# Performance work log

Measured on AMD Instinct MI355X. Metric: run time of the kernel, lower is better.

## Reference

```python
import jax, jax.numpy as jnp
import numpy as np

DIMS, K_SIZE, V_SIZE, SEQ_LEN = 1024, 128, 128, 2048
MINUS = -100.0


def setup_inputs() -> dict:
    key = jax.random.key(0)
    k1, k2, k3, k4, k5 = jax.random.split(key, 5)
    B, S = 8, 2048
    minibatch = jax.random.normal(k1, (B, S, DIMS), dtype=jnp.float32)
    # Linear params (torch nn.Linear default init scale ~ U(-1/sqrt(fan_in), ...)); use scaled normals
    s = 1.0 / np.sqrt(DIMS)
    Wk = jax.random.normal(k2, (DIMS, K_SIZE), dtype=jnp.float32) * s
    bk = jax.random.normal(k3, (K_SIZE,), dtype=jnp.float32) * s
    Wv = jax.random.normal(k4, (DIMS, V_SIZE), dtype=jnp.float32) * s
    bv = jax.random.normal(k5, (V_SIZE,), dtype=jnp.float32) * s
    return {"minibatch": minibatch, "Wk": Wk, "bk": bk, "Wv": Wv, "bv": bv,
            "current_seq_len": S}


def reference(minibatch, Wk, bk, Wv, bv, current_seq_len):
    # keys == queries (shared projection, as in the original forward)
    keys = minibatch @ Wk + bk              # [B,S,K]
    values = minibatch @ Wv + bv            # [B,S,V]
    S = current_seq_len
    mask = jnp.tril(jnp.ones((S, S), dtype=jnp.float32))  # [S,S] lower-triangular
    scores = jnp.einsum('bsk,btk->bst', keys, keys) / np.sqrt(K_SIZE)
    logits = mask * scores + MINUS * (1.0 - mask)
    probs = jax.nn.softmax(logits, axis=2)
    read = jnp.einsum('bst,btv->bsv', probs, values)  # [B,S,V]
    return jnp.concatenate([minibatch, read], axis=2)  # [B,S,dims+V]
```

## Files before the change

kernel.cpp:

```cpp
#include <hip/hip_runtime.h>
#include <hip/hip_bf16.h>

#define BATCH 8
#define SEQ   2048
#define DMS   1024
#define KSZ   128
#define OD    1152

typedef unsigned short u16;
typedef unsigned int   u32;
typedef __attribute__((ext_vector_type(4)))  float  f32x4;
typedef __attribute__((ext_vector_type(16))) float  f32x16;
typedef __attribute__((ext_vector_type(8)))  __bf16 bf16x8;

union U128 { uint4 u4; bf16x8 b8; u16 us[8]; u32 u[4]; };

__device__ inline u16 f2bf(float f) {
  union { __bf16 h; u16 u; } c;
  c.h = (__bf16)f;
  return c.u;
}

__device__ inline float fexp2(float x) {
  float r;
  asm("v_exp_f32 %0, %1" : "=v"(r) : "v"(x));
  return r;
}

__device__ inline f32x4 mfma16(bf16x8 a, bf16x8 b, f32x4 c) {
  return __builtin_amdgcn_mfma_f32_16x16x32_bf16(a, b, c, 0, 0, 0);
}
__device__ inline f32x16 mfma32(bf16x8 a, bf16x8 b, f32x16 c) {
  return __builtin_amdgcn_mfma_f32_32x32x16_bf16(a, b, c, 0, 0, 0);
}

#define BSTRIDE 262144

__global__ void __launch_bounds__(256) prep_kernel(
    const float* __restrict__ Wk, const float* __restrict__ Wv,
    u16* __restrict__ Wtiles)
{
  int T = blockIdx.x * 256 + threadIdx.x;
  int n  = T & 255;
  int kc = (T >> 8) * 8;
  int ks = kc >> 6;
  int kk = kc & 63;
  const float* src = (n < 128) ? (Wk + n) : (Wv + (n - 128));
  U128 w;
#pragma unroll
  for (int j = 0; j < 8; ++j) w.us[j] = f2bf(src[(size_t)(kc + j) * KSZ]);
  u16* dst = Wtiles + ks * 16384 + n * 64 + (kk ^ ((n & 7) << 3));
  *(uint4*)dst = w.u4;
}

__global__ void __launch_bounds__(256, 2) proj_kernel(
    const float* __restrict__ X, const u16* __restrict__ Wtiles,
    const float* __restrict__ bk, const float* __restrict__ bv,
    float* __restrict__ out, u16* __restrict__ Kfrag, u16* __restrict__ Vfrag)
{
  __shared__ u16 Ab[32 * 64];
  __shared__ u16 Bt[256 * 64];

  const int tid  = threadIdx.x;
  const int lane = tid & 63;
  const int wid  = tid >> 6;
  const int l15  = lane & 15;
  const int g    = lane >> 4;
  const int m0   = blockIdx.x * 32;

  const int ar = tid >> 3;
  const int ac = (tid & 7) * 8;

  f32x4 acc[2][4];
#pragma unroll
  for (int i = 0; i < 2; ++i)
#pragma unroll
    for (int j = 0; j < 4; ++j) acc[i][j] = (f32x4){0.f, 0.f, 0.f, 0.f};

  char* AbB = (char*)Ab;
  char* BtB = (char*)Bt;

  for (int ks = 0; ks < 16; ++ks) {
    __syncthreads();
    {
      const float* xp = X + (size_t)(m0 + ar) * DMS + ks * 64 + ac;
      float4 a0 = *(const float4*)xp;
      float4 a1 = *(const float4*)(xp + 4);
      float* op = out + (size_t)(m0 + ar) * OD + ks * 64 + ac;
      *(float4*)op = a0;
      *(float4*)(op + 4) = a1;
      U128 w;
      w.us[0] = f2bf(a0.x); w.us[1] = f2bf(a0.y);
      w.us[2] = f2bf(a0.z); w.us[3] = f2bf(a0.w);
      w.us[4] = f2bf(a1.x); w.us[5] = f2bf(a1.y);
      w.us[6] = f2bf(a1.z); w.us[7] = f2bf(a1.w);
      int ab = (ar * 128 + ac * 2) ^ ((ar & 7) << 4);
      *(uint4*)(AbB + ab) = w.u4;
    }
    {
      const u16* wsrc = Wtiles + (size_t)ks * 16384 + wid * 4096 + lane * 8;
#pragma unroll
      for (int i = 0; i < 8; ++i) {
        __builtin_amdgcn_global_load_lds(
            (const __attribute__((address_space(1))) u32*)(wsrc + i * 512),
            (__attribute__((address_space(3))) u32*)(Bt + wid * 4096 + i * 512),
            16, 0, 0);
      }
    }
    __syncthreads();
#pragma unroll
    for (int kh = 0; kh < 2; ++kh) {
      bf16x8 af[2], bfr[4];
#pragma unroll
      for (int mf = 0; mf < 2; ++mf) {
        int m = mf * 16 + l15;
        int ab = (m * 128 + (kh * 32 + g * 8) * 2) ^ ((m & 7) << 4);
        U128 u; u.u4 = *(uint4*)(AbB + ab); af[mf] = u.b8;
      }
#pragma unroll
      for (int nf = 0; nf < 4; ++nf) {
        int n = wid * 64 + nf * 16 + l15;
        int bb = (n * 128 + (kh * 32 + g * 8) * 2) ^ ((n & 7) << 4);
        U128 u; u.u4 = *(uint4*)(BtB + bb); bfr[nf] = u.b8;
      }
#pragma unroll
      for (int mf = 0; mf < 2; ++mf)
#pragma unroll
        for (int nf = 0; nf < 4; ++nf)
          acc[mf][nf] = mfma16(af[mf], bfr[nf], acc[mf][nf]);
    }
  }

  __syncthreads();
#pragma unroll
  for (int nf = 0; nf < 4; ++nf) {
    int n = wid * 64 + nf * 16 + l15;
    float bias = (n < 128) ? bk[n] : bv[n - 128];
#pragma unroll
    for (int mf = 0; mf < 2; ++mf)
#pragma unroll
      for (int j = 0; j < 4; ++j) {
        int s = mf * 16 + g * 4 + j;
        Bt[s * 256 + (n ^ ((s & 7) << 3))] = f2bf(acc[mf][nf][j] + bias);
      }
  }
  __syncthreads();

  const int bb   = m0 >> 11;
  const int tloc = (m0 & 2047) >> 5;

  {
    int sl = tid >> 3;
    int ks = tid & 7;
    u16* dst = Kfrag + (size_t)bb * BSTRIDE + (size_t)(tloc * 8 + ks) * 512 + sl * 8;
#pragma unroll
    for (int hi2 = 0; hi2 < 2; ++hi2) {
      int n = ks * 16 + hi2 * 8;
      uint4 v = *(const uint4*)&Bt[sl * 256 + (n ^ ((sl & 7) << 3))];
      *(uint4*)(dst + hi2 * 256) = v;
    }
  }
  {
    int l31 = tid & 31;
    int vb2 = (tid >> 5) & 3;
    int th  = tid >> 7;
    int n   = 128 + vb2 * 32 + l31;
    u16* dst = Vfrag + (size_t)bb * BSTRIDE +
               (size_t)((tloc * 4 + vb2) * 2 + th) * 512 + l31 * 8;
#pragma unroll
    for (int hi = 0; hi < 2; ++hi) {
      U128 w;
#pragma unroll
      for (int j = 0; j < 8; ++j) {
        int s = th * 16 + hi * 8 + j;
        w.us[j] = Bt[s * 256 + (n ^ ((s & 7) << 3))];
      }
      *(uint4*)(dst + hi * 256) = w.u4;
    }
  }
}

__global__ void __launch_bounds__(256, 2) attn_kernel(
    const u16* __restrict__ Kfrag, const u16* __restrict__ Vfrag,
    float* __restrict__ out)
{
  __shared__ float Om[4][128][33];
  __shared__ float Ml[4][2][32];
  __shared__ float Wm[4][32];
  __shared__ float Li[32];

  const int tid  = threadIdx.x;
  const int lane = tid & 63;
  const int w    = tid >> 6;
  const int l31  = lane & 31;
  const int hi   = lane >> 5;

  const int bi = blockIdx.x;
  const int b  = bi & 7;
  const int qt = (bi < 256) ? (63 - (bi >> 3)) : ((bi >> 3) - 32);
  const int q0 = qt * 32;

  const u16* Kb = Kfrag + (size_t)b * BSTRIDE;
  const u16* Vb = Vfrag + (size_t)b * BSTRIDE;
  const int loff = hi * 256 + l31 * 8;

  bf16x8 qf[8];
  {
    const u16* qp = Kb + (size_t)(qt * 8) * 512 + loff;
#pragma unroll
    for (int ks = 0; ks < 8; ++ks) {
      U128 u; u.u4 = *(const uint4*)(qp + ks * 512); qf[ks] = u.b8;
    }
  }

  f32x16 o[4];
#pragma unroll
  for (int vb2 = 0; vb2 < 4; ++vb2)
#pragma unroll
    for (int i = 0; i < 16; ++i) o[vb2][i] = 0.f;

  float mrun = -3.0e38f, lsum = 0.f;
  const float SC  = 0.08838834764831845f;
  const float L2E = 1.44269504088896341f;

  bf16x8 kf[8];
  {
    int ti0 = (w <= qt) ? w : 0;
    const u16* kp = Kb + (size_t)(ti0 * 8) * 512 + loff;
#pragma unroll
    for (int ks = 0; ks < 8; ++ks) {
      U128 u; u.u4 = *(const uint4*)(kp + ks * 512); kf[ks] = u.b8;
    }
  }

  for (int ti = w; ti <= qt; ti += 4) {
    bf16x8 vf[4][2];
    {
      const u16* vp = Vb + (size_t)(ti * 8) * 512 + loff;
#pragma unroll
      for (int vb2 = 0; vb2 < 4; ++vb2)
#pragma unroll
        for (int th = 0; th < 2; ++th) {
          U128 u; u.u4 = *(const uint4*)(vp + (vb2 * 2 + th) * 512);
          vf[vb2][th] = u.b8;
        }
    }
    f32x16 s;
#pragma unroll
    for (int i = 0; i < 16; ++i) s[i] = 0.f;
#pragma unroll
    for (int ks = 0; ks < 8; ++ks) s = mfma32(kf[ks], qf[ks], s);
    {
      int tin = (ti + 4 <= qt) ? ti + 4 : ti;
      const u16* kp = Kb + (size_t)(tin * 8) * 512 + loff;
#pragma unroll
      for (int ks = 0; ks < 8; ++ks) {
        U128 u; u.u4 = *(const uint4*)(kp + ks * 512); kf[ks] = u.b8;
      }
    }
    float sv[16];
#pragma unroll
    for (int r = 0; r < 16; ++r) sv[r] = s[r] * SC;
    if (ti == qt) {
#pragma unroll
      for (int r = 0; r < 16; ++r) {
        int toff = (r & 3) + 8 * (r >> 2) + 4 * hi;
        if (toff > l31) sv[r] = -3.0e38f;
      }
    }
    float mx = sv[0];
#pragma unroll
    for (int r = 1; r < 16; ++r) mx = fmaxf(mx, sv[r]);
    mx = fmaxf(mx, __shfl_xor(mx, 32));
    float p[16];
    float ps = 0.f;
    if (__all(mx - mrun <= 8.0f)) {
#pragma unroll
      for (int r = 0; r < 16; ++r) { p[r] = fexp2((sv[r] - mrun) * L2E); ps += p[r]; }
      ps += __shfl_xor(ps, 32);
      lsum += ps;
    } else {
      float mnew = fmaxf(mrun, mx);
      float al = fexp2((mrun - mnew) * L2E);
#pragma unroll
      for (int r = 0; r < 16; ++r) { p[r] = fexp2((sv[r] - mnew) * L2E); ps += p[r]; }
      ps += __shfl_xor(ps, 32);
      lsum = lsum * al + ps;
      mrun = mnew;
#pragma unroll
      for (int vb2 = 0; vb2 < 4; ++vb2)
#pragma unroll
        for (int i = 0; i < 16; ++i) o[vb2][i] *= al;
    }
    u32 c01 = (u32)f2bf(p[0])  | ((u32)f2bf(p[1])  << 16);
    u32 c23 = (u32)f2bf(p[2])  | ((u32)f2bf(p[3])  << 16);
    u32 c45 = (u32)f2bf(p[4])  | ((u32)f2bf(p[5])  << 16);
    u32 c67 = (u32)f2bf(p[6])  | ((u32)f2bf(p[7])  << 16);
    u32 c89 = (u32)f2bf(p[8])  | ((u32)f2bf(p[9])  << 16);
    u32 cAB = (u32)f2bf(p[10]) | ((u32)f2bf(p[11]) << 16);
    u32 cCD = (u32)f2bf(p[12]) | ((u32)f2bf(p[13]) << 16);
    u32 cEF = (u32)f2bf(p[14]) | ((u32)f2bf(p[15]) << 16);
    u32 d01 = __shfl_xor(c01, 32);
    u32 d23 = __shfl_xor(c23, 32);
    u32 d45 = __shfl_xor(c45, 32);
    u32 d67 = __shfl_xor(c67, 32);
    u32 d89 = __shfl_xor(c89, 32);
    u32 dAB = __shfl_xor(cAB, 32);
    u32 dCD = __shfl_xor(cCD, 32);
    u32 dEF = __shfl_xor(cEF, 32);
    U128 pf1, pf2;
    pf1.u[0] = hi ? d45 : c01;
    pf1.u[1] = hi ? d67 : c23;
    pf1.u[2] = hi ? c45 : d01;
    pf1.u[3] = hi ? c67 : d23;
    pf2.u[0] = hi ? dCD : c89;
    pf2.u[1] = hi ? dEF : cAB;
    pf2.u[2] = hi ? cCD : d89;
    pf2.u[3] = hi ? cEF : dAB;
#pragma unroll
    for (int vb2 = 0; vb2 < 4; ++vb2) {
      o[vb2] = mfma32(vf[vb2][0], pf1.b8, o[vb2]);
      o[vb2] = mfma32(vf[vb2][1], pf2.b8, o[vb2]);
    }
  }

#pragma unroll
  for (int vb2 = 0; vb2 < 4; ++vb2)
#pragma unroll
    for (int r = 0; r < 16; ++r) {
      int v = vb2 * 32 + (r & 3) + 8 * (r >> 2) + 4 * hi;
      Om[w][v][l31] = o[vb2][r];
    }
  if (lane < 32) {
    Ml[w][0][l31] = mrun;
    Ml[w][1][l31] = lsum;
  }
  __syncthreads();

  if (tid < 32) {
    float m0 = Ml[0][0][tid], m1 = Ml[1][0][tid];
    float m2 = Ml[2][0][tid], m3 = Ml[3][0][tid];
    float M  = fmaxf(fmaxf(m0, m1), fmaxf(m2, m3));
    float w0 = fexp2((m0 - M) * L2E), w1 = fexp2((m1 - M) * L2E);
    float w2 = fexp2((m2 - M) * L2E), w3 = fexp2((m3 - M) * L2E);
    float L  = Ml[0][1][tid] * w0 + Ml[1][1][tid] * w1 +
               Ml[2][1][tid] * w2 + Ml[3][1][tid] * w3;
    Wm[0][tid] = w0; Wm[1][tid] = w1; Wm[2][tid] = w2; Wm[3][tid] = w3;
    Li[tid] = 1.f / L;
  }
  __syncthreads();

  {
    const int q = tid >> 3;
    const int vbase = (tid & 7) * 16;
    float wq0 = Wm[0][q], wq1 = Wm[1][q], wq2 = Wm[2][q], wq3 = Wm[3][q];
    float li = Li[q];
    float* orow = out + (size_t)(b * SEQ + q0 + q) * OD + 1024 + vbase;
#pragma unroll
    for (int i = 0; i < 16; i += 4) {
      float4 res;
      res.x = (Om[0][vbase + i + 0][q] * wq0 + Om[1][vbase + i + 0][q] * wq1 +
               Om[2][vbase + i + 0][q] * wq2 + Om[3][vbase + i + 0][q] * wq3) * li;
      res.y = (Om[0][vbase + i + 1][q] * wq0 + Om[1][vbase + i + 1][q] * wq1 +
               Om[2][vbase + i + 1][q] * wq2 + Om[3][vbase + i + 1][q] * wq3) * li;
      res.z = (Om[0][vbase + i + 2][q] * wq0 + Om[1][vbase + i + 2][q] * wq1 +
               Om[2][vbase + i + 2][q] * wq2 + Om[3][vbase + i + 2][q] * wq3) * li;
      res.w = (Om[0][vbase + i + 3][q] * wq0 + Om[1][vbase + i + 3][q] * wq1 +
               Om[2][vbase + i + 3][q] * wq2 + Om[3][vbase + i + 3][q] * wq3) * li;
      *(float4*)(orow + i) = res;
    }
  }
}

extern "C" void kernel_launch(void* const* d_in, const int* in_sizes, int n_in,
                              void* d_out, int out_size, void* d_ws, size_t ws_size,
                              hipStream_t stream)
{
  const float* X  = (const float*)d_in[0];
  const float* Wk = (const float*)d_in[1];
  const float* bk = (const float*)d_in[2];
  const float* Wv = (const float*)d_in[3];
  const float* bv = (const float*)d_in[4];
  float* out = (float*)d_out;

  u16* Kfrag  = (u16*)d_ws;
  u16* Vfrag  = Kfrag + (size_t)BATCH * BSTRIDE;
  u16* Wtiles = Vfrag + (size_t)BATCH * BSTRIDE;

  prep_kernel<<<dim3(128), dim3(256), 0, stream>>>(Wk, Wv, Wtiles);
  proj_kernel<<<dim3(512), dim3(256), 0, stream>>>(X, Wtiles, bk, bv, out, Kfrag, Vfrag);
  attn_kernel<<<dim3(512), dim3(256), 0, stream>>>(Kfrag, Vfrag, out);
}
```

Before: 67.36 us.

## Double-buffer projection GEMM and widen tile to 64 rows with 8 waves

Rewrites the projection kernel to use 512 threads and 64-row tiles, so each block loads the weight tile once for twice as many rows. It double-buffers the X and W tiles in LDS, prefetching step k+1 while step k runs its MFMAs, and needs only one barrier per K-step. The aim is to hide global-load latency and halve weight-tile traffic. In exchange, LDS use is larger and the grid drops to 256 blocks, which may leave CUs idle on a 256-CU part or reduce occupancy.

```diff
diff --git a/kernel.cpp b/kernel.cpp
--- a/kernel.cpp
+++ b/kernel.cpp
@@ -32,6 +32,21 @@
 }
 __device__ inline f32x16 mfma32(bf16x8 a, bf16x8 b, f32x16 c) {
   return __builtin_amdgcn_mfma_f32_32x32x16_bf16(a, b, c, 0, 0, 0);
+}
+
+__device__ inline uint4 pack8bf(float4 a, float4 b) {
+  U128 w;
+  w.us[0] = f2bf(a.x); w.us[1] = f2bf(a.y);
+  w.us[2] = f2bf(a.z); w.us[3] = f2bf(a.w);
+  w.us[4] = f2bf(b.x); w.us[5] = f2bf(b.y);
+  w.us[6] = f2bf(b.z); w.us[7] = f2bf(b.w);
+  return w.u4;
+}
+
+__device__ inline void glds16(const u16* src, u16* ldsDst) {
+  __builtin_amdgcn_global_load_lds(
+      (const __attribute__((address_space(1))) u32*)src,
+      (__attribute__((address_space(3))) u32*)ldsDst, 16, 0, 0);
 }
 
 #define BSTRIDE 262144
@@ -53,74 +68,78 @@
   *(uint4*)dst = w.u4;
 }
 
-__global__ void __launch_bounds__(256, 2) proj_kernel(
+__global__ void __launch_bounds__(512, 1) proj_kernel(
     const float* __restrict__ X, const u16* __restrict__ Wtiles,
     const float* __restrict__ bk, const float* __restrict__ bv,
     float* __restrict__ out, u16* __restrict__ Kfrag, u16* __restrict__ Vfrag)
 {
-  __shared__ u16 Ab[32 * 64];
-  __shared__ u16 Bt[256 * 64];
+  __shared__ u16 Ab[2][64 * 64];
+  __shared__ u16 Bt[2][256 * 64];
 
   const int tid  = threadIdx.x;
   const int lane = tid & 63;
-  const int wid  = tid >> 6;
+  const int wv   = tid >> 6;
+  const int wm   = wv >> 2;
+  const int wn   = wv & 3;
   const int l15  = lane & 15;
   const int g    = lane >> 4;
-  const int m0   = blockIdx.x * 32;
+  const int m0   = blockIdx.x * 64;
 
   const int ar = tid >> 3;
   const int ac = (tid & 7) * 8;
 
+  const float* xrow = X + (size_t)(m0 + ar) * DMS + ac;
+  float*       orow = out + (size_t)(m0 + ar) * OD + ac;
+  const int   abOff = (ar * 128 + ac * 2) ^ ((ar & 7) << 4);
+
+  char* AbB = (char*)&Ab[0][0];
+  char* BtB = (char*)&Bt[0][0];
+
   f32x4 acc[2][4];
 #pragma unroll
   for (int i = 0; i < 2; ++i)
 #pragma unroll
     for (int j = 0; j < 4; ++j) acc[i][j] = (f32x4){0.f, 0.f, 0.f, 0.f};
 
-  char* AbB = (char*)Ab;
-  char* BtB = (char*)Bt;
-
-  for (int ks = 0; ks < 16; ++ks) {
-    __syncthreads();
-    {
-      const float* xp = X + (size_t)(m0 + ar) * DMS + ks * 64 + ac;
-      float4 a0 = *(const float4*)xp;
-      float4 a1 = *(const float4*)(xp + 4);
-      float* op = out + (size_t)(m0 + ar) * OD + ks * 64 + ac;
-      *(float4*)op = a0;
-      *(float4*)(op + 4) = a1;
-      U128 w;
-      w.us[0] = f2bf(a0.x); w.us[1] = f2bf(a0.y);
-      w.us[2] = f2bf(a0.z); w.us[3] = f2bf(a0.w);
-      w.us[4] = f2bf(a1.x); w.us[5] = f2bf(a1.y);
-      w.us[6] = f2bf(a1.z); w.us[7] = f2bf(a1.w);
-      int ab = (ar * 128 + ac * 2) ^ ((ar & 7) << 4);
-      *(uint4*)(AbB + ab) = w.u4;
-    }
-    {
-      const u16* wsrc = Wtiles + (size_t)ks * 16384 + wid * 4096 + lane * 8;
-#pragma unroll
-      for (int i = 0; i < 8; ++i) {
-        __builtin_amdgcn_global_load_lds(
-            (const __attribute__((address_space(1))) u32*)(wsrc + i * 512),
-            (__attribute__((address_space(3))) u32*)(Bt + wid * 4096 + i * 512),
-            16, 0, 0);
-      }
-    }
-    __syncthreads();
+  float4 xv[2][2];
+
+  xv[0][0] = *(const float4*)(xrow);
+  xv[0][1] = *(const float4*)(xrow + 4);
+  {
+    const u16* ws = Wtiles + wv * 512 + lane * 8;
+    u16* wd = &Bt[0][0] + wv * 512;
+#pragma unroll
+    for (int r = 0; r < 4; ++r) glds16(ws + r * 4096, wd + r * 4096);
+  }
+  *(uint4*)(AbB + abOff) = pack8bf(xv[0][0], xv[0][1]);
+  __syncthreads();
+
+#pragma unroll
+  for (int k = 0; k < 16; ++k) {
+    const int cur = k & 1, nxt = cur ^ 1;
+    *(float4*)(orow + k * 64)     = xv[cur][0];
+    *(float4*)(orow + k * 64 + 4) = xv[cur][1];
+    if (k < 15) {
+      xv[nxt][0] = *(const float4*)(xrow + (k + 1) * 64);
+      xv[nxt][1] = *(const float4*)(xrow + (k + 1) * 64 + 4);
+      const u16* ws = Wtiles + (size_t)(k + 1) * 16384 + wv * 512 + lane * 8;
+      u16* wd = &Bt[nxt][0] + wv * 512;
+#pragma unroll
+      for (int r = 0; r < 4; ++r) glds16(ws + r * 4096, wd + r * 4096);
+    }
 #pragma unroll
     for (int kh = 0; kh < 2; ++kh) {
       bf16x8 af[2], bfr[4];
 #pragma unroll
       for (int mf = 0; mf < 2; ++mf) {
-        int m = mf * 16 + l15;
-        int ab = (m * 128 + (kh * 32 + g * 8) * 2) ^ ((m & 7) << 4);
+        int m = wm * 32 + mf * 16 + l15;
+        int ab = cur * 8192 + ((m * 128 + (kh * 32 + g * 8) * 2) ^ ((m & 7) << 4));
         U128 u; u.u4 = *(uint4*)(AbB + ab); af[mf] = u.b8;
       }
 #pragma unroll
       for (int nf = 0; nf < 4; ++nf) {
-        int n = wid * 64 + nf * 16 + l15;
-        int bb = (n * 128 + (kh * 32 + g * 8) * 2) ^ ((n & 7) << 4);
+        int n = wn * 64 + nf * 16 + l15;
+        int bb = cur * 32768 + ((n * 128 + (kh * 32 + g * 8) * 2) ^ ((n & 7) << 4));
         U128 u; u.u4 = *(uint4*)(BtB + bb); bfr[nf] = u.b8;
       }
 #pragma unroll
@@ -129,51 +148,58 @@
         for (int nf = 0; nf < 4; ++nf)
           acc[mf][nf] = mfma16(af[mf], bfr[nf], acc[mf][nf]);
     }
-  }
-
+    if (k < 15)
+      *(uint4*)(AbB + nxt * 8192 + abOff) = pack8bf(xv[nxt][0], xv[nxt][1]);
+    __syncthreads();
+  }
+
+  u16* Ct = &Bt[0][0];
+#pragma unroll
+  for (int nf = 0; nf < 4; ++nf) {
+    int n = wn * 64 + nf * 16 + l15;
+    float bias = (n < 128) ? bk[n] : bv[n - 128];
+#pragma unroll
+    for (int mf = 0; mf < 2; ++mf)
+#pragma unroll
+      for (int j = 0; j < 4; ++j) {
+        int s = wm * 32 + mf * 16 + g * 4 + j;
+        Ct[s * 256 + (n ^ ((s & 7) << 3))] = f2bf(acc[mf][nf][j] + bias);
+      }
+  }
   __syncthreads();
-#pragma unroll
-  for (int nf = 0; nf < 4; ++nf) {
-    int n = wid * 64 + nf * 16 + l15;
-    float bias = (n < 128) ? bk[n] : bv[n - 128];
-#pragma unroll
-    for (int mf = 0; mf < 2; ++mf)
-#pragma unroll
-      for (int j = 0; j < 4; ++j) {
-        int s = mf * 16 + g * 4 + j;
-        Bt[s * 256 + (n ^ ((s & 7) << 3))] = f2bf(acc[mf][nf][j] + bias);
-      }
-  }
-  __syncthreads();
-
-  const int bb   = m0 >> 11;
-  const int tloc = (m0 & 2047) >> 5;
+
+  const int bb    = m0 >> 11;
+  const int tloc2 = (m0 & 2047) >> 5;
 
   {
     int sl = tid >> 3;
     int ks = tid & 7;
-    u16* dst = Kfrag + (size_t)bb * BSTRIDE + (size_t)(tloc * 8 + ks) * 512 + sl * 8;
+    int t2 = tloc2 + (sl >> 5);
+    int lrow = sl & 31;
+    u16* dst = Kfrag + (size_t)bb * BSTRIDE + (size_t)(t2 * 8 + ks) * 512 + lrow * 8;
 #pragma unroll
     for (int hi2 = 0; hi2 < 2; ++hi2) {
       int n = ks * 16 + hi2 * 8;
-      uint4 v = *(const uint4*)&Bt[sl * 256 + (n ^ ((sl & 7) << 3))];
+      uint4 v = *(const uint4*)&Ct[sl * 256 + (n ^ ((sl & 7) << 3))];
       *(uint4*)(dst + hi2 * 256) = v;
     }
   }
   {
     int l31 = tid & 31;
     int vb2 = (tid >> 5) & 3;
-    int th  = tid >> 7;
+    int thh = (tid >> 7) & 1;
+    int sh2 = tid >> 8;
+    int t2  = tloc2 + sh2;
     int n   = 128 + vb2 * 32 + l31;
     u16* dst = Vfrag + (size_t)bb * BSTRIDE +
-               (size_t)((tloc * 4 + vb2) * 2 + th) * 512 + l31 * 8;
+               (size_t)((t2 * 4 + vb2) * 2 + thh) * 512 + l31 * 8;
 #pragma unroll
     for (int hi = 0; hi < 2; ++hi) {
       U128 w;
 #pragma unroll
       for (int j = 0; j < 8; ++j) {
-        int s = th * 16 + hi * 8 + j;
-        w.us[j] = Bt[s * 256 + (n ^ ((s & 7) << 3))];
+        int s = sh2 * 32 + thh * 16 + hi * 8 + j;
+        w.us[j] = Ct[s * 256 + (n ^ ((s & 7) << 3))];
       }
       *(uint4*)(dst + hi * 256) = w.u4;
     }
@@ -388,6 +414,6 @@
   u16* Wtiles = Vfrag + (size_t)BATCH * BSTRIDE;
 
   prep_kernel<<<dim3(128), dim3(256), 0, stream>>>(Wk, Wv, Wtiles);
-  proj_kernel<<<dim3(512), dim3(256), 0, stream>>>(X, Wtiles, bk, bv, out, Kfrag, Vfrag);
+  proj_kernel<<<dim3(256), dim3(512), 0, stream>>>(X, Wtiles, bk, bv, out, Kfrag, Vfrag);
   attn_kernel<<<dim3(512), dim3(256), 0, stream>>>(Kfrag, Vfrag, out);
 }
```

Measured after the change: 67.17 us. No clear change (-0.3%).

## Restructure projection to per-wave register GEMM with pre-fragmented weights

Applied to the files above, without the earlier changes.

The weight prep kernel now writes W directly in MFMA B-fragment order, so the projection kernel loads B operands straight from global memory (L2) into registers, with no LDS staging and no block-wide barriers in the K loop. Each wave owns a 16-row by 128-column tile (K half or V half), converts X rows to bf16 in registers, and prefetches the next X chunk. LDS is now used only per wave for the epilogue transpose. In exchange, X is read twice (once per column half) and every wave streams the weights from L2 rather than sharing an LDS copy.

```diff
diff --git a/kernel.cpp b/kernel.cpp
--- a/kernel.cpp
+++ b/kernel.cpp
@@ -34,148 +34,135 @@
   return __builtin_amdgcn_mfma_f32_32x32x16_bf16(a, b, c, 0, 0, 0);
 }
 
+__device__ inline uint4 pack8bf(float4 a, float4 b) {
+  U128 w;
+  w.us[0] = f2bf(a.x); w.us[1] = f2bf(a.y);
+  w.us[2] = f2bf(a.z); w.us[3] = f2bf(a.w);
+  w.us[4] = f2bf(b.x); w.us[5] = f2bf(b.y);
+  w.us[6] = f2bf(b.z); w.us[7] = f2bf(b.w);
+  return w.u4;
+}
+
 #define BSTRIDE 262144
+
 
 __global__ void __launch_bounds__(256) prep_kernel(
     const float* __restrict__ Wk, const float* __restrict__ Wv,
-    u16* __restrict__ Wtiles)
+    u16* __restrict__ Wfrag)
 {
   int T = blockIdx.x * 256 + threadIdx.x;
-  int n  = T & 255;
-  int kc = (T >> 8) * 8;
-  int ks = kc >> 6;
-  int kk = kc & 63;
+  int lane = T & 63;
+  int nf   = (T >> 6) & 15;
+  int ks   = T >> 10;
+  int l15  = lane & 15;
+  int g    = lane >> 4;
+  int n    = nf * 16 + l15;
   const float* src = (n < 128) ? (Wk + n) : (Wv + (n - 128));
+  int k0 = ks * 32 + g * 8;
   U128 w;
 #pragma unroll
-  for (int j = 0; j < 8; ++j) w.us[j] = f2bf(src[(size_t)(kc + j) * KSZ]);
-  u16* dst = Wtiles + ks * 16384 + n * 64 + (kk ^ ((n & 7) << 3));
-  *(uint4*)dst = w.u4;
-}
-
-__global__ void __launch_bounds__(256, 2) proj_kernel(
-    const float* __restrict__ X, const u16* __restrict__ Wtiles,
+  for (int j = 0; j < 8; ++j) w.us[j] = f2bf(src[(size_t)(k0 + j) * KSZ]);
+  *(uint4*)(Wfrag + (size_t)T * 8) = w.u4;
+}
+
+__global__ void __launch_bounds__(256) proj_kernel(
+    const float* __restrict__ X, const u16* __restrict__ Wfrag,
     const float* __restrict__ bk, const float* __restrict__ bv,
     float* __restrict__ out, u16* __restrict__ Kfrag, u16* __restrict__ Vfrag)
 {
-  __shared__ u16 Ab[32 * 64];
-  __shared__ u16 Bt[256 * 64];
+  __shared__ u16 Ct[4][16 * 128];
 
   const int tid  = threadIdx.x;
   const int lane = tid & 63;
-  const int wid  = tid >> 6;
+  const int w    = tid >> 6;
   const int l15  = lane & 15;
   const int g    = lane >> 4;
-  const int m0   = blockIdx.x * 32;
-
-  const int ar = tid >> 3;
-  const int ac = (tid & 7) * 8;
-
-  f32x4 acc[2][4];
-#pragma unroll
-  for (int i = 0; i < 2; ++i)
-#pragma unroll
-    for (int j = 0; j < 4; ++j) acc[i][j] = (f32x4){0.f, 0.f, 0.f, 0.f};
-
-  char* AbB = (char*)Ab;
-  char* BtB = (char*)Bt;
-
-  for (int ks = 0; ks < 16; ++ks) {
-    __syncthreads();
-    {
-      const float* xp = X + (size_t)(m0 + ar) * DMS + ks * 64 + ac;
-      float4 a0 = *(const float4*)xp;
-      float4 a1 = *(const float4*)(xp + 4);
-      float* op = out + (size_t)(m0 + ar) * OD + ks * 64 + ac;
-      *(float4*)op = a0;
-      *(float4*)(op + 4) = a1;
-      U128 w;
-      w.us[0] = f2bf(a0.x); w.us[1] = f2bf(a0.y);
-      w.us[2] = f2bf(a0.z); w.us[3] = f2bf(a0.w);
-      w.us[4] = f2bf(a1.x); w.us[5] = f2bf(a1.y);
-      w.us[6] = f2bf(a1.z); w.us[7] = f2bf(a1.w);
-      int ab = (ar * 128 + ac * 2) ^ ((ar & 7) << 4);
-      *(uint4*)(AbB + ab) = w.u4;
-    }
-    {
-      const u16* wsrc = Wtiles + (size_t)ks * 16384 + wid * 4096 + lane * 8;
-#pragma unroll
-      for (int i = 0; i < 8; ++i) {
-        __builtin_amdgcn_global_load_lds(
-            (const __attribute__((address_space(1))) u32*)(wsrc + i * 512),
-            (__attribute__((address_space(3))) u32*)(Bt + wid * 4096 + i * 512),
-            16, 0, 0);
+
+  const int gw = blockIdx.x * 4 + w;
+  const int rt = gw >> 1;
+  const int nh = gw & 1;
+  const int m0 = rt * 16;
+
+  const float* xrow = X + (size_t)(m0 + l15) * DMS + g * 8;
+  float*       orow = out + (size_t)(m0 + l15) * OD + g * 8;
+  const u16*   wbase = Wfrag + (size_t)(nh * 8) * 512 + lane * 8;
+
+  f32x4 acc[8];
+#pragma unroll
+  for (int nf = 0; nf < 8; ++nf) acc[nf] = (f32x4){0.f, 0.f, 0.f, 0.f};
+
+  float4 a0 = *(const float4*)(xrow);
+  float4 a1 = *(const float4*)(xrow + 4);
+
+#pragma unroll 2
+  for (int ks = 0; ks < 32; ++ks) {
+    float4 n0, n1;
+    if (ks < 31) {
+      n0 = *(const float4*)(xrow + (ks + 1) * 32);
+      n1 = *(const float4*)(xrow + (ks + 1) * 32 + 4);
+    }
+    if (nh == 0) {
+      *(float4*)(orow + ks * 32)     = a0;
+      *(float4*)(orow + ks * 32 + 4) = a1;
+    }
+    U128 aw; aw.u4 = pack8bf(a0, a1);
+    const u16* bp = wbase + (size_t)ks * 8192;
+#pragma unroll
+    for (int nf = 0; nf < 8; ++nf) {
+      U128 u; u.u4 = *(const uint4*)(bp + nf * 512);
+      acc[nf] = mfma16(aw.b8, u.b8, acc[nf]);
+    }
+    a0 = n0; a1 = n1;
+  }
+
+  const float* bias_src = nh ? bv : bk;
+  u16* C = &Ct[w][0];
+#pragma unroll
+  for (int nf = 0; nf < 8; ++nf) {
+    float bs = bias_src[nf * 16 + l15];
+#pragma unroll
+    for (int j = 0; j < 4; ++j) {
+      int r = g * 4 + j;
+      C[r * 128 + ((nf * 16 + l15) ^ ((r & 7) << 3))] = f2bf(acc[nf][j] + bs);
+    }
+  }
+
+  const int b  = m0 >> 11;
+  const int t2 = (m0 & 2047) >> 5;
+  const int rb = m0 & 16;
+
+  if (nh == 0) {
+#pragma unroll
+    for (int h = 0; h < 2; ++h) {
+      int r   = (lane >> 3) + 8 * h;
+      int ks2 = lane & 7;
+      int l31 = rb + r;
+      u16* dst = Kfrag + (size_t)b * BSTRIDE + (size_t)(t2 * 8 + ks2) * 512 + l31 * 8;
+#pragma unroll
+      for (int hi2 = 0; hi2 < 2; ++hi2) {
+        uint4 v = *(const uint4*)&C[r * 128 + ((ks2 * 16 + hi2 * 8) ^ ((r & 7) << 3))];
+        *(uint4*)(dst + hi2 * 256) = v;
       }
     }
-    __syncthreads();
-#pragma unroll
-    for (int kh = 0; kh < 2; ++kh) {
-      bf16x8 af[2], bfr[4];
-#pragma unroll
-      for (int mf = 0; mf < 2; ++mf) {
-        int m = mf * 16 + l15;
-        int ab = (m * 128 + (kh * 32 + g * 8) * 2) ^ ((m & 7) << 4);
-        U128 u; u.u4 = *(uint4*)(AbB + ab); af[mf] = u.b8;
+  } else {
+    const int th   = rb >> 4;
+    const int l31v = lane & 31;
+    const int vbs  = lane >> 5;
+#pragma unroll
+    for (int t = 0; t < 2; ++t) {
+      int vb2 = vbs + t * 2;
+#pragma unroll
+      for (int hi = 0; hi < 2; ++hi) {
+        U128 wv;
+#pragma unroll
+        for (int j = 0; j < 8; ++j) {
+          int r = hi * 8 + j;
+          wv.us[j] = C[r * 128 + ((vb2 * 32 + l31v) ^ ((r & 7) << 3))];
+        }
+        u16* dst = Vfrag + (size_t)b * BSTRIDE +
+                   (size_t)((t2 * 4 + vb2) * 2 + th) * 512 + hi * 256 + l31v * 8;
+        *(uint4*)dst = wv.u4;
       }
-#pragma unroll
-      for (int nf = 0; nf < 4; ++nf) {
-        int n = wid * 64 + nf * 16 + l15;
-        int bb = (n * 128 + (kh * 32 + g * 8) * 2) ^ ((n & 7) << 4);
-        U128 u; u.u4 = *(uint4*)(BtB + bb); bfr[nf] = u.b8;
-      }
-#pragma unroll
-      for (int mf = 0; mf < 2; ++mf)
-#pragma unroll
-        for (int nf = 0; nf < 4; ++nf)
-          acc[mf][nf] = mfma16(af[mf], bfr[nf], acc[mf][nf]);
-    }
-  }
-
-  __syncthreads();
-#pragma unroll
-  for (int nf = 0; nf < 4; ++nf) {
-    int n = wid * 64 + nf * 16 + l15;
-    float bias = (n < 128) ? bk[n] : bv[n - 128];
-#pragma unroll
-    for (int mf = 0; mf < 2; ++mf)
-#pragma unroll
-      for (int j = 0; j < 4; ++j) {
-        int s = mf * 16 + g * 4 + j;
-        Bt[s * 256 + (n ^ ((s & 7) << 3))] = f2bf(acc[mf][nf][j] + bias);
-      }
-  }
-  __syncthreads();
-
-  const int bb   = m0 >> 11;
-  const int tloc = (m0 & 2047) >> 5;
-
-  {
-    int sl = tid >> 3;
-    int ks = tid & 7;
-    u16* dst = Kfrag + (size_t)bb * BSTRIDE + (size_t)(tloc * 8 + ks) * 512 + sl * 8;
-#pragma unroll
-    for (int hi2 = 0; hi2 < 2; ++hi2) {
-      int n = ks * 16 + hi2 * 8;
-      uint4 v = *(const uint4*)&Bt[sl * 256 + (n ^ ((sl & 7) << 3))];
-      *(uint4*)(dst + hi2 * 256) = v;
-    }
-  }
-  {
-    int l31 = tid & 31;
-    int vb2 = (tid >> 5) & 3;
-    int th  = tid >> 7;
-    int n   = 128 + vb2 * 32 + l31;
-    u16* dst = Vfrag + (size_t)bb * BSTRIDE +
-               (size_t)((tloc * 4 + vb2) * 2 + th) * 512 + l31 * 8;
-#pragma unroll
-    for (int hi = 0; hi < 2; ++hi) {
-      U128 w;
-#pragma unroll
-      for (int j = 0; j < 8; ++j) {
-        int s = th * 16 + hi * 8 + j;
-        w.us[j] = Bt[s * 256 + (n ^ ((s & 7) << 3))];
-      }
-      *(uint4*)(dst + hi * 256) = w.u4;
     }
   }
 }
@@ -383,11 +370,11 @@
   const float* bv = (const float*)d_in[4];
   float* out = (float*)d_out;
 
-  u16* Kfrag  = (u16*)d_ws;
-  u16* Vfrag  = Kfrag + (size_t)BATCH * BSTRIDE;
-  u16* Wtiles = Vfrag + (size_t)BATCH * BSTRIDE;
-
-  prep_kernel<<<dim3(128), dim3(256), 0, stream>>>(Wk, Wv, Wtiles);
-  proj_kernel<<<dim3(512), dim3(256), 0, stream>>>(X, Wtiles, bk, bv, out, Kfrag, Vfrag);
+  u16* Kfrag = (u16*)d_ws;
+  u16* Vfrag = Kfrag + (size_t)BATCH * BSTRIDE;
+  u16* Wfrag = Vfrag + (size_t)BATCH * BSTRIDE;
+
+  prep_kernel<<<dim3(128), dim3(256), 0, stream>>>(Wk, Wv, Wfrag);
+  proj_kernel<<<dim3(512), dim3(256), 0, stream>>>(X, Wfrag, bk, bv, out, Kfrag, Vfrag);
   attn_kernel<<<dim3(512), dim3(256), 0, stream>>>(Kfrag, Vfrag, out);
 }
```

Measured after the change: 91.17 us. +35.3%, slower.
